# Performance work log

Hardware: AMD Instinct MI355X
Metric: run time of the kernel (lower is better)

The kernel has to match this reference:

```python
import jax, jax.numpy as jnp
import numpy as np

T, E, IN_F, OUT_F = 16384, 8, 2048, 4096


def setup_inputs() -> dict:
    key = jax.random.key(0)
    k1, k2 = jax.random.split(key)
    input_tokens = jax.random.normal(k1, (T, IN_F), dtype=jnp.float32)
    # weight_stack[e] is [out_features, in_features]; forward does x_e @ W_e.T
    weight_stack = jax.random.normal(k2, (E, OUT_F, IN_F), dtype=jnp.float32) * (1.0 / np.sqrt(IN_F))
    # tokens are pre-sorted by expert; sizes must sum to total_tokens
    m_sizes = jnp.full((E,), T // E, dtype=jnp.int32)
    m_offsets = jnp.concatenate([
        jnp.zeros((1,), jnp.int32),
        jnp.cumsum(m_sizes)[:-1].astype(jnp.int32),
    ])
    return {
        "input_tokens": input_tokens,
        "weight_stack": weight_stack,
        "m_sizes": m_sizes,
        "m_offsets": m_offsets,
    }


def reference(input_tokens, weight_stack, m_sizes, m_offsets):
    # Grouped GEMM: for expert e, rows [off_e : off_e + m_e] of the output are
    #   input_tokens[off_e : off_e + m_e] @ weight_stack[e].T
    # lax.ragged_dot expects rhs of shape [groups, K, N]; weight_stack is [E, N, K],
    # so a stride-only swapaxes gives the logical transpose (no data movement),
    # mirroring the CUTLASS stride-based transpose avoidance.
    rhs = jnp.swapaxes(weight_stack, 1, 2)  # [E, in_features, out_features]
    out = jax.lax.ragged_dot(input_tokens, rhs, m_sizes)  # [T, out_features]
    return out
```

## Files before the change

kernel.cpp:

```cpp
#include <hip/hip_runtime.h>
#include <hip/hip_bf16.h>
#include <stdint.h>

#define T_TOK 16384
#define NEXP  8
#define KF    2048
#define NF    4096

#define BM  256
#define BN  256
#define BKT 64
#define KT  (KF / BKT)

typedef __bf16 bf16;
typedef __attribute__((ext_vector_type(8))) __bf16  bf16x8;
typedef __attribute__((ext_vector_type(4))) __bf16  bf16x4;
typedef __attribute__((ext_vector_type(4))) float   f32x4;

__device__ __forceinline__ void async_copy16(const void* g, void* l) {
  __builtin_amdgcn_global_load_lds(
      (const __attribute__((address_space(1))) void*)g,
      (__attribute__((address_space(3))) void*)l,
      16, 0, 0);
}

__global__ __launch_bounds__(256) void convert_f32_to_bf16(
    const float* __restrict__ in, bf16* __restrict__ out, int n8) {
  int i = blockIdx.x * 256 + threadIdx.x;
  if (i >= n8) return;
  const float4* p = (const float4*)(in + (size_t)i * 8);
  float4 a = p[0];
  float4 b = p[1];
  bf16x8 v;
  v[0] = (bf16)a.x; v[1] = (bf16)a.y; v[2] = (bf16)a.z; v[3] = (bf16)a.w;
  v[4] = (bf16)b.x; v[5] = (bf16)b.y; v[6] = (bf16)b.z; v[7] = (bf16)b.w;
  *(bf16x8*)(out + (size_t)i * 8) = v;
}

__global__ __launch_bounds__(512, 2) void grouped_gemm_pipe(
    const bf16* __restrict__ Xb, const bf16* __restrict__ Wb,
    const int* __restrict__ m_offsets, float* __restrict__ out)
{
  __shared__ bf16 As[2][BM * BKT];
  __shared__ bf16 Bs[2][BN * BKT];

  const int bid = blockIdx.x;
  const int swz = (bid & 7) * 128 + (bid >> 3);
  const int m0 = (swz >> 4) * BM;
  const int n0 = (swz & 15) * BN;

  int e = 0;
#pragma unroll
  for (int i = 1; i < NEXP; ++i)
    if (m0 >= m_offsets[i]) e = i;

  const int tid  = threadIdx.x;
  const int lane = tid & 63;
  const int wave = tid >> 6;
  const int wm = (wave >> 2) * 128;
  const int wn = (wave & 3) * 64;
  const int q  = lane >> 4;
  const int r  = lane & 15;

  const bf16* Ag = Xb + (size_t)m0 * KF;
  const bf16* Bg = Wb + ((size_t)e * NF + n0) * KF;

  const int crow = tid >> 3;
  const int cbs  = (((tid & 7) << 4) ^ ((crow & 7) << 4));

#define STAGE_A(BUF, H, TT) do {                                              \
    const bf16* _s = Ag + (size_t)((H) * 128 + crow) * KF + (TT) * BKT        \
                        + (cbs >> 1);                                         \
    char* _d = (char*)(&As[(BUF)][(H) * 128 * BKT]) + tid * 16;               \
    async_copy16(_s, _d);                                                     \
    async_copy16(_s + (size_t)64 * KF, _d + 8192);                            \
  } while (0)
#define STAGE_B(BUF, H, TT) do {                                              \
    const bf16* _s = Bg + (size_t)((H) * 128 + crow) * KF + (TT) * BKT        \
                        + (cbs >> 1);                                         \
    char* _d = (char*)(&Bs[(BUF)][(H) * 128 * BKT]) + tid * 16;               \
    async_copy16(_s, _d);                                                     \
    async_copy16(_s + (size_t)64 * KF, _d + 8192);                            \
  } while (0)

  f32x4 acc[8][4];
#pragma unroll
  for (int m = 0; m < 8; ++m)
#pragma unroll
    for (int n = 0; n < 4; ++n)
      acc[m][n] = (f32x4)0.0f;

  STAGE_A(0, 0, 0); STAGE_A(0, 1, 0); STAGE_B(0, 0, 0); STAGE_B(0, 1, 0);
  STAGE_B(1, 0, 1); STAGE_B(1, 1, 1);
  asm volatile("s_waitcnt vmcnt(4)" ::: "memory");
  __builtin_amdgcn_s_barrier();
  __builtin_amdgcn_sched_barrier(0);

#pragma unroll 2
  for (int t = 0; t < KT; ++t) {
    const int buf = t & 1;
    const char* Ab = (const char*)&As[buf][0];
    const char* Bb = (const char*)&Bs[buf][0];
    bf16x8 b0[4], b1[4], a0[4], a1[4];

#pragma unroll
    for (int n = 0; n < 4; ++n) {
      const int row = wn + n * 16 + r;
      b0[n] = *(const bf16x8*)(Bb + row * 128 + ((q * 16) ^ ((row & 7) << 4)));
    }
#pragma unroll
    for (int m = 0; m < 4; ++m) {
      const int row = wm + m * 16 + r;
      a0[m] = *(const bf16x8*)(Ab + row * 128 + ((q * 16) ^ ((row & 7) << 4)));
    }
    __builtin_amdgcn_sched_barrier(0);
#pragma unroll
    for (int n = 0; n < 4; ++n) {
      const int row = wn + n * 16 + r;
      b1[n] = *(const bf16x8*)(Bb + row * 128 + ((64 + q * 16) ^ ((row & 7) << 4)));
    }
#pragma unroll
    for (int m = 0; m < 4; ++m) {
      const int row = wm + 64 + m * 16 + r;
      a1[m] = *(const bf16x8*)(Ab + row * 128 + ((q * 16) ^ ((row & 7) << 4)));
    }
    if (t + 1 < KT) { STAGE_A(buf ^ 1, 0, t + 1); STAGE_A(buf ^ 1, 1, t + 1); }

    asm volatile("s_waitcnt lgkmcnt(8)" ::: "memory");
    __builtin_amdgcn_sched_barrier(0);
    __builtin_amdgcn_s_setprio(1);
#pragma unroll
    for (int m = 0; m < 4; ++m)
#pragma unroll
      for (int n = 0; n < 4; ++n)
        acc[m][n] = __builtin_amdgcn_mfma_f32_16x16x32_bf16(
            a0[m], b0[n], acc[m][n], 0, 0, 0);
    __builtin_amdgcn_s_setprio(0);
    __builtin_amdgcn_sched_barrier(0);

#pragma unroll
    for (int m = 0; m < 4; ++m) {
      const int row = wm + m * 16 + r;
      a0[m] = *(const bf16x8*)(Ab + row * 128 + ((64 + q * 16) ^ ((row & 7) << 4)));
    }
    asm volatile("s_waitcnt lgkmcnt(4)" ::: "memory");
    __builtin_amdgcn_sched_barrier(0);
    __builtin_amdgcn_s_setprio(1);
#pragma unroll
    for (int m = 0; m < 4; ++m)
#pragma unroll
      for (int n = 0; n < 4; ++n)
        acc[4 + m][n] = __builtin_amdgcn_mfma_f32_16x16x32_bf16(
            a1[m], b0[n], acc[4 + m][n], 0, 0, 0);
    __builtin_amdgcn_s_setprio(0);
    __builtin_amdgcn_sched_barrier(0);

#pragma unroll
    for (int m = 0; m < 4; ++m) {
      const int row = wm + 64 + m * 16 + r;
      a1[m] = *(const bf16x8*)(Ab + row * 128 + ((64 + q * 16) ^ ((row & 7) << 4)));
    }
    asm volatile("s_waitcnt lgkmcnt(4)" ::: "memory");
    __builtin_amdgcn_sched_barrier(0);
    __builtin_amdgcn_s_setprio(1);
#pragma unroll
    for (int m = 0; m < 4; ++m)
#pragma unroll
      for (int n = 0; n < 4; ++n)
        acc[m][n] = __builtin_amdgcn_mfma_f32_16x16x32_bf16(
            a0[m], b1[n], acc[m][n], 0, 0, 0);
    __builtin_amdgcn_s_setprio(0);

    __builtin_amdgcn_s_barrier();
    if (t + 2 < KT) { STAGE_B(buf, 0, t + 2); STAGE_B(buf, 1, t + 2); }

    asm volatile("s_waitcnt lgkmcnt(0)" ::: "memory");
    __builtin_amdgcn_sched_barrier(0);
    __builtin_amdgcn_s_setprio(1);
#pragma unroll
    for (int m = 0; m < 4; ++m)
#pragma unroll
      for (int n = 0; n < 4; ++n)
        acc[4 + m][n] = __builtin_amdgcn_mfma_f32_16x16x32_bf16(
            a1[m], b1[n], acc[4 + m][n], 0, 0, 0);
    __builtin_amdgcn_s_setprio(0);

    if (t + 1 < KT) {
      if (t + 2 < KT) { asm volatile("s_waitcnt vmcnt(4)" ::: "memory"); }
      else            { asm volatile("s_waitcnt vmcnt(0)" ::: "memory"); }
      __builtin_amdgcn_s_barrier();
      __builtin_amdgcn_sched_barrier(0);
    }
  }
#undef STAGE_A
#undef STAGE_B

#pragma unroll
  for (int m = 0; m < 8; ++m) {
#pragma unroll
    for (int n = 0; n < 4; ++n) {
      const int col = n0 + wn + n * 16 + r;
#pragma unroll
      for (int rr = 0; rr < 4; ++rr) {
        const int row = m0 + wm + m * 16 + q * 4 + rr;
        out[(size_t)row * NF + col] = acc[m][n][rr];
      }
    }
  }
}

__global__ __launch_bounds__(256) void grouped_gemm_bt_f32(
    const float* __restrict__ Xf, const float* __restrict__ Wf,
    const int* __restrict__ m_offsets, float* __restrict__ out)
{
  __shared__ bf16 As[128 * 32];
  __shared__ bf16 Bs[128 * 32];

  const int n0 = blockIdx.x * 128;
  const int m0 = blockIdx.y * 128;

  int e = 0;
#pragma unroll
  for (int i = 1; i < NEXP; ++i)
    if (m0 >= m_offsets[i]) e = i;

  const int tid  = threadIdx.x;
  const int lane = tid & 63;
  const int wave = tid >> 6;
  const int wm = (wave >> 1) * 64;
  const int wn = (wave & 1) * 64;
  const int q  = lane >> 4;
  const int r  = lane & 15;

  f32x4 acc[4][4];
#pragma unroll
  for (int im = 0; im < 4; ++im)
#pragma unroll
    for (int in = 0; in < 4; ++in)
      acc[im][in] = (f32x4)0.0f;

  const float* Af = Xf + (size_t)m0 * KF;
  const float* Bf = Wf + ((size_t)e * NF + n0) * KF;

  for (int kt = 0; kt < KF / 32; ++kt) {
#pragma unroll
    for (int i = 0; i < 4; ++i) {
      int f   = (i * 256 + tid) * 4;
      int row = f >> 5;
      int kel = f & 31;
      float4 av = *(const float4*)(Af + (size_t)row * KF + kt * 32 + kel);
      float4 bv = *(const float4*)(Bf + (size_t)row * KF + kt * 32 + kel);
      bf16x4 a4, b4;
      a4[0] = (bf16)av.x; a4[1] = (bf16)av.y; a4[2] = (bf16)av.z; a4[3] = (bf16)av.w;
      b4[0] = (bf16)bv.x; b4[1] = (bf16)bv.y; b4[2] = (bf16)bv.z; b4[3] = (bf16)bv.w;
      *(bf16x4*)(As + f) = a4;
      *(bf16x4*)(Bs + f) = b4;
    }
    __syncthreads();

    bf16x8 afr[4], bfr[4];
#pragma unroll
    for (int im = 0; im < 4; ++im)
      afr[im] = *(const bf16x8*)&As[(wm + im * 16 + r) * 32 + q * 8];
#pragma unroll
    for (int in = 0; in < 4; ++in)
      bfr[in] = *(const bf16x8*)&Bs[(wn + in * 16 + r) * 32 + q * 8];

#pragma unroll
    for (int im = 0; im < 4; ++im)
#pragma unroll
      for (int in = 0; in < 4; ++in)
        acc[im][in] = __builtin_amdgcn_mfma_f32_16x16x32_bf16(
            afr[im], bfr[in], acc[im][in], 0, 0, 0);

    __syncthreads();
  }

#pragma unroll
  for (int im = 0; im < 4; ++im) {
#pragma unroll
    for (int in = 0; in < 4; ++in) {
      int col = n0 + wn + in * 16 + r;
#pragma unroll
      for (int rr = 0; rr < 4; ++rr) {
        int row = m0 + wm + im * 16 + q * 4 + rr;
        out[(size_t)row * NF + col] = acc[im][in][rr];
      }
    }
  }
}

extern "C" void kernel_launch(void* const* d_in, const int* in_sizes, int n_in,
                              void* d_out, int out_size, void* d_ws, size_t ws_size,
                              hipStream_t stream) {
  const float* X         = (const float*)d_in[0];
  const float* W         = (const float*)d_in[1];
  const int*   m_offsets = (const int*)d_in[3];
  float*       out       = (float*)d_out;

  const size_t xElems = (size_t)T_TOK * KF;
  const size_t wElems = (size_t)NEXP * NF * KF;
  const size_t needed = (xElems + wElems) * sizeof(bf16);

  if (ws_size >= needed) {
    bf16* Xb = (bf16*)d_ws;
    bf16* Wb = (bf16*)((char*)d_ws + xElems * sizeof(bf16));
    int n8x = (int)(xElems / 8);
    int n8w = (int)(wElems / 8);
    convert_f32_to_bf16<<<n8x / 256, 256, 0, stream>>>(X, Xb, n8x);
    convert_f32_to_bf16<<<n8w / 256, 256, 0, stream>>>(W, Wb, n8w);
    dim3 grid((T_TOK / BM) * (NF / BN));
    grouped_gemm_pipe<<<grid, 512, 0, stream>>>(Xb, Wb, m_offsets, out);
  } else {
    dim3 grid(NF / 128, T_TOK / 128);
    grouped_gemm_bt_f32<<<grid, 256, 0, stream>>>(
        X, W, m_offsets, out);
  }
}
```

Measured before the change: 776.9 us.

## Precompute LDS fragment pointers and interleave loads with barriers around MFMA phases

Replaces the separate A/B shared arrays with one raw LDS buffer and precomputes per-lane swizzled fragment pointers, so per-iteration address arithmetic drops to constant offsets. Each of the four MFMA phases now loads only its own fragments, then takes a workgroup barrier and a full lgkmcnt(0) wait before the MFMAs. The intent is to keep waves in lockstep, ping-pong style, so LDS reads and MFMA work from the two co-resident blocks interleave. The extra barriers and full waits remove the old partial-wait overlap of LDS reads with MFMAs and could add stall time.

```diff
diff --git a/kernel.cpp b/kernel.cpp
--- a/kernel.cpp
+++ b/kernel.cpp
@@ -37,12 +37,11 @@
   *(bf16x8*)(out + (size_t)i * 8) = v;
 }
 
-__global__ __launch_bounds__(512, 2) void grouped_gemm_pipe(
+__global__ __launch_bounds__(512, 2) void grouped_gemm_m201(
     const bf16* __restrict__ Xb, const bf16* __restrict__ Wb,
     const int* __restrict__ m_offsets, float* __restrict__ out)
 {
-  __shared__ bf16 As[2][BM * BKT];
-  __shared__ bf16 Bs[2][BN * BKT];
+  __shared__ __align__(16) char smem[131072];
 
   const int bid = blockIdx.x;
   const int swz = (bid & 7) * 128 + (bid >> 3);
@@ -71,17 +70,31 @@
 #define STAGE_A(BUF, H, TT) do {                                              \
     const bf16* _s = Ag + (size_t)((H) * 128 + crow) * KF + (TT) * BKT        \
                         + (cbs >> 1);                                         \
-    char* _d = (char*)(&As[(BUF)][(H) * 128 * BKT]) + tid * 16;               \
+    char* _d = smem + (BUF) * 32768 + (H) * 16384 + tid * 16;                 \
     async_copy16(_s, _d);                                                     \
     async_copy16(_s + (size_t)64 * KF, _d + 8192);                            \
   } while (0)
 #define STAGE_B(BUF, H, TT) do {                                              \
     const bf16* _s = Bg + (size_t)((H) * 128 + crow) * KF + (TT) * BKT        \
                         + (cbs >> 1);                                         \
-    char* _d = (char*)(&Bs[(BUF)][(H) * 128 * BKT]) + tid * 16;               \
+    char* _d = smem + 65536 + (BUF) * 32768 + (H) * 16384 + tid * 16;         \
     async_copy16(_s, _d);                                                     \
     async_copy16(_s + (size_t)64 * KF, _d + 8192);                            \
   } while (0)
+
+  const int swc = (lane & 7) << 4;
+  const int ca  = (q * 16) ^ swc;
+  const int cb  = (64 + q * 16) ^ swc;
+  const char* pA0[2], * pA1[2], * pB0[2], * pB1[2];
+#pragma unroll
+  for (int b = 0; b < 2; ++b) {
+    const char* Abase = smem + b * 32768 + (wm + r) * 128;
+    const char* Bbase = smem + 65536 + b * 32768 + (wn + r) * 128;
+    pA0[b] = Abase + ca;
+    pA1[b] = Abase + cb;
+    pB0[b] = Bbase + ca;
+    pB1[b] = Bbase + cb;
+  }
 
   f32x4 acc[8][4];
 #pragma unroll
@@ -99,34 +112,17 @@
 #pragma unroll 2
   for (int t = 0; t < KT; ++t) {
     const int buf = t & 1;
-    const char* Ab = (const char*)&As[buf][0];
-    const char* Bb = (const char*)&Bs[buf][0];
     bf16x8 b0[4], b1[4], a0[4], a1[4];
 
 #pragma unroll
-    for (int n = 0; n < 4; ++n) {
-      const int row = wn + n * 16 + r;
-      b0[n] = *(const bf16x8*)(Bb + row * 128 + ((q * 16) ^ ((row & 7) << 4)));
-    }
-#pragma unroll
-    for (int m = 0; m < 4; ++m) {
-      const int row = wm + m * 16 + r;
-      a0[m] = *(const bf16x8*)(Ab + row * 128 + ((q * 16) ^ ((row & 7) << 4)));
-    }
-    __builtin_amdgcn_sched_barrier(0);
-#pragma unroll
-    for (int n = 0; n < 4; ++n) {
-      const int row = wn + n * 16 + r;
-      b1[n] = *(const bf16x8*)(Bb + row * 128 + ((64 + q * 16) ^ ((row & 7) << 4)));
-    }
-#pragma unroll
-    for (int m = 0; m < 4; ++m) {
-      const int row = wm + 64 + m * 16 + r;
-      a1[m] = *(const bf16x8*)(Ab + row * 128 + ((q * 16) ^ ((row & 7) << 4)));
-    }
+    for (int n = 0; n < 4; ++n)
+      b0[n] = *(const bf16x8*)(pB0[buf] + n * 2048);
+#pragma unroll
+    for (int m = 0; m < 4; ++m)
+      a0[m] = *(const bf16x8*)(pA0[buf] + m * 2048);
     if (t + 1 < KT) { STAGE_A(buf ^ 1, 0, t + 1); STAGE_A(buf ^ 1, 1, t + 1); }
-
-    asm volatile("s_waitcnt lgkmcnt(8)" ::: "memory");
+    __builtin_amdgcn_s_barrier();
+    asm volatile("s_waitcnt lgkmcnt(0)" ::: "memory");
     __builtin_amdgcn_sched_barrier(0);
     __builtin_amdgcn_s_setprio(1);
 #pragma unroll
@@ -136,14 +132,13 @@
         acc[m][n] = __builtin_amdgcn_mfma_f32_16x16x32_bf16(
             a0[m], b0[n], acc[m][n], 0, 0, 0);
     __builtin_amdgcn_s_setprio(0);
-    __builtin_amdgcn_sched_barrier(0);
-
-#pragma unroll
-    for (int m = 0; m < 4; ++m) {
-      const int row = wm + m * 16 + r;
-      a0[m] = *(const bf16x8*)(Ab + row * 128 + ((64 + q * 16) ^ ((row & 7) << 4)));
-    }
-    asm volatile("s_waitcnt lgkmcnt(4)" ::: "memory");
+    __builtin_amdgcn_s_barrier();
+
+#pragma unroll
+    for (int m = 0; m < 4; ++m)
+      a1[m] = *(const bf16x8*)(pA0[buf] + 8192 + m * 2048);
+    __builtin_amdgcn_s_barrier();
+    asm volatile("s_waitcnt lgkmcnt(0)" ::: "memory");
     __builtin_amdgcn_sched_barrier(0);
     __builtin_amdgcn_s_setprio(1);
 #pragma unroll
@@ -153,14 +148,16 @@
         acc[4 + m][n] = __builtin_amdgcn_mfma_f32_16x16x32_bf16(
             a1[m], b0[n], acc[4 + m][n], 0, 0, 0);
     __builtin_amdgcn_s_setprio(0);
-    __builtin_amdgcn_sched_barrier(0);
-
-#pragma unroll
-    for (int m = 0; m < 4; ++m) {
-      const int row = wm + 64 + m * 16 + r;
-      a1[m] = *(const bf16x8*)(Ab + row * 128 + ((64 + q * 16) ^ ((row & 7) << 4)));
-    }
-    asm volatile("s_waitcnt lgkmcnt(4)" ::: "memory");
+    __builtin_amdgcn_s_barrier();
+
+#pragma unroll
+    for (int n = 0; n < 4; ++n)
+      b1[n] = *(const bf16x8*)(pB1[buf] + n * 2048);
+#pragma unroll
+    for (int m = 0; m < 4; ++m)
+      a0[m] = *(const bf16x8*)(pA1[buf] + m * 2048);
+    __builtin_amdgcn_s_barrier();
+    asm volatile("s_waitcnt lgkmcnt(0)" ::: "memory");
     __builtin_amdgcn_sched_barrier(0);
     __builtin_amdgcn_s_setprio(1);
 #pragma unroll
@@ -170,10 +167,13 @@
         acc[m][n] = __builtin_amdgcn_mfma_f32_16x16x32_bf16(
             a0[m], b1[n], acc[m][n], 0, 0, 0);
     __builtin_amdgcn_s_setprio(0);
-
-    __builtin_amdgcn_s_barrier();
+    __builtin_amdgcn_s_barrier();
+
+#pragma unroll
+    for (int m = 0; m < 4; ++m)
+      a1[m] = *(const bf16x8*)(pA1[buf] + 8192 + m * 2048);
     if (t + 2 < KT) { STAGE_B(buf, 0, t + 2); STAGE_B(buf, 1, t + 2); }
-
+    __builtin_amdgcn_s_barrier();
     asm volatile("s_waitcnt lgkmcnt(0)" ::: "memory");
     __builtin_amdgcn_sched_barrier(0);
     __builtin_amdgcn_s_setprio(1);
@@ -310,7 +310,7 @@
     convert_f32_to_bf16<<<n8x / 256, 256, 0, stream>>>(X, Xb, n8x);
     convert_f32_to_bf16<<<n8w / 256, 256, 0, stream>>>(W, Wb, n8w);
     dim3 grid((T_TOK / BM) * (NF / BN));
-    grouped_gemm_pipe<<<grid, 512, 0, stream>>>(Xb, Wb, m_offsets, out);
+    grouped_gemm_m201<<<grid, 512, 0, stream>>>(Xb, Wb, m_offsets, out);
   } else {
     dim3 grid(NF / 128, T_TOK / 128);
     grouped_gemm_bt_f32<<<grid, 256, 0, stream>>>(
```

Result: faster. 761.2 us (-2.0%).
